# Optimization experiments

Measured on AMD Instinct MI355X. Metric: run time of the kernel, lower is better.

Reference implementation:

```python
import jax, jax.numpy as jnp
import numpy as np

BATCH = 8
HIDDEN = 256          # per-head size == input channels
NUM_HEADS = 9
H_IMG = 48
W_IMG = 48


def make_R(w, h):
    """Relative-position feature tensor R[i,j,k,l] = [dx, dy, dx^2, dy^2, dx*dy]
    with dx = k - i, dy = l - j (matches torch.meshgrid indexing='ij')."""
    gx, gy = jnp.meshgrid(jnp.arange(w), jnp.arange(h), indexing='ij')
    grid = jnp.stack([gx, gy], axis=-1).astype(jnp.float32)        # (w,h,2)
    rel = grid[None, None, :, :, :] - grid[:, :, None, None, :]    # (w,h,w,h,2)
    return jnp.concatenate(
        [rel, rel ** 2, (rel[..., 0] * rel[..., 1])[..., None]], axis=-1
    )                                                              # (w,h,w,h,5)


def setup_inputs() -> dict:
    key = jax.random.key(0)
    k1, k2, k3, k4, k5 = jax.random.split(key, 5)
    hidden_states = jax.random.normal(k1, (BATCH, HIDDEN, H_IMG, W_IMG), dtype=jnp.float32)
    # init per module: centers ~ N(0, init_mu_std=2.0), spreads = 1 + N(0, 0.01)
    attention_centers = 2.0 * jax.random.normal(k2, (NUM_HEADS, 2), dtype=jnp.float32)
    attention_spreads = 1.0 + 0.01 * jax.random.normal(k3, (NUM_HEADS,), dtype=jnp.float32)
    value_w = 0.02 * jax.random.normal(k4, (HIDDEN, NUM_HEADS * HIDDEN), dtype=jnp.float32)
    value_b = 0.02 * jax.random.normal(k5, (HIDDEN,), dtype=jnp.float32)
    return {
        'hidden_states': hidden_states,
        'attention_centers': attention_centers,
        'attention_spreads': attention_spreads,
        'value_w': value_w,
        'value_b': value_b,
    }


def reference(hidden_states, attention_centers, attention_spreads, value_w, value_b):
    b, c, h, w = hidden_states.shape
    x = jnp.transpose(hidden_states, (0, 3, 2, 1))  # (b, w, h, c)

    # heads target vectors (isotropic gaussian): a = c = sigma^2, b = 0
    a = attention_spreads ** 2                       # (H,)
    mu1 = attention_centers[:, 0]
    mu2 = attention_centers[:, 1]
    # t_h = -1/2 * [-2 a mu1, -2 a mu2, a, a, 0] = [a mu1, a mu2, -a/2, -a/2, 0]
    u = jnp.stack([a * mu1, a * mu2, -0.5 * a, -0.5 * a, jnp.zeros_like(a)], axis=-1)  # (H,5)

    R = make_R(w, h)                                               # (w,h,w,h,5)
    scores = jnp.einsum('ijkld,hd->ijhkl', R, u)                   # (w,h,H,w,h)
    probs = jax.nn.softmax(scores.reshape(w, h, NUM_HEADS, -1), axis=-1)
    probs = probs.reshape(w, h, NUM_HEADS, w, h)
    # dropout is identity in eval mode

    vals = jnp.einsum('ijhkl,bkld->bijhd', probs, x)               # (b,w,h,H,c)
    vals = vals.reshape(b, w, h, NUM_HEADS * c)
    out = vals @ value_w.T + value_b                               # (b,w,h,hidden)
    out = jnp.transpose(out, (0, 3, 2, 1))                         # (b,hidden,h,w)
    return out, probs
```

## Files before the change

### kernel.cpp

```cpp
#include <hip/hip_runtime.h>
#include <cstdint>
#include <cstddef>

#define SS    2304
#define OUT0  4718592

typedef short bf16x8 __attribute__((ext_vector_type(8)));
typedef float f32x4  __attribute__((ext_vector_type(4)));

__device__ __forceinline__ unsigned short f2bf(float f) {
    union { float f; unsigned int i; } v; v.f = f;
    unsigned int x = v.i;
    unsigned int r = x + 0x7fffu + ((x >> 16) & 1u);
    return (unsigned short)(r >> 16);
}

__global__ __launch_bounds__(256) void k_pre(const float* __restrict__ centers,
                                             const float* __restrict__ spreads,
                                             const float* __restrict__ hs,
                                             const float* __restrict__ Wv,
                                             float* __restrict__ p1, float* __restrict__ p2,
                                             unsigned short* __restrict__ p1b,
                                             unsigned short* __restrict__ p2b,
                                             unsigned short* __restrict__ hsb,
                                             unsigned short* __restrict__ WF) {
    int blk = blockIdx.x;
    int t = threadIdx.x;
    if (blk < 108) {
        int lane = t & 63, wave = t >> 6;
        int ridx = blk * 4 + wave;
        int h = ridx / 48, r = ridx % 48;
        float a = spreads[h]; a = a * a;
        float mu1 = centers[2 * h + 0];
        float mu2 = centers[2 * h + 1];
        bool act = lane < 48;
        float dx = (float)(lane - r);
        float q  = -0.5f * a * dx * dx;
        float g1 = act ? (a * mu1 * dx + q) : -INFINITY;
        float g2 = act ? (a * mu2 * dx + q) : -INFINITY;
        float m1 = g1, m2 = g2;
        #pragma unroll
        for (int off = 32; off >= 1; off >>= 1) {
            m1 = fmaxf(m1, __shfl_xor(m1, off));
            m2 = fmaxf(m2, __shfl_xor(m2, off));
        }
        float e1 = act ? expf(g1 - m1) : 0.f;
        float e2 = act ? expf(g2 - m2) : 0.f;
        float s1 = e1, s2 = e2;
        #pragma unroll
        for (int off = 32; off >= 1; off >>= 1) {
            s1 += __shfl_xor(s1, off);
            s2 += __shfl_xor(s2, off);
        }
        float v1 = e1 / s1, v2 = e2 / s2;
        if (act) {
            p1[h * SS + r * 48 + lane] = v1;
            p2[h * SS + r * 48 + lane] = v2;
        }
        p1b[(h * 48 + r) * 64 + lane] = act ? f2bf(v1) : 0;
        p2b[(h * 48 + r) * 64 + lane] = act ? f2bf(v2) : 0;
    } else if (blk < 396) {
        int kb = blk - 108;
        int e  = t;
        const float* src = Wv + (size_t)e * 2304 + kb * 8;
        float4 f0 = *(const float4*)src;
        float4 f1 = *(const float4*)(src + 4);
        uint4 o;
        o.x = (unsigned int)f2bf(f0.x) | ((unsigned int)f2bf(f0.y) << 16);
        o.y = (unsigned int)f2bf(f0.z) | ((unsigned int)f2bf(f0.w) << 16);
        o.z = (unsigned int)f2bf(f1.x) | ((unsigned int)f2bf(f1.y) << 16);
        o.w = (unsigned int)f2bf(f1.z) | ((unsigned int)f2bf(f1.w) << 16);
        *(uint4*)(WF + ((size_t)kb * 256 + e) * 8) = o;
    } else {
        int bd = blk - 396;
        const float* src = hs + (size_t)bd * SS;
        unsigned short* dst = hsb + (size_t)bd * 3072;
        for (int u = t; u < 384; u += 256) {
            int l = u >> 3, c8 = u & 7;
            uint4 o = {0u, 0u, 0u, 0u};
            if (c8 < 6) {
                const float* p = src + l * 48 + c8 * 8;
                float4 f0 = *(const float4*)p;
                float4 f1 = *(const float4*)(p + 4);
                o.x = (unsigned int)f2bf(f0.x) | ((unsigned int)f2bf(f0.y) << 16);
                o.y = (unsigned int)f2bf(f0.z) | ((unsigned int)f2bf(f0.w) << 16);
                o.z = (unsigned int)f2bf(f1.x) | ((unsigned int)f2bf(f1.y) << 16);
                o.w = (unsigned int)f2bf(f1.z) | ((unsigned int)f2bf(f1.w) << 16);
            }
            *(uint4*)(dst + l * 64 + c8 * 8) = o;
        }
    }
}

__global__ __launch_bounds__(256, 3) void k_attn(const unsigned short* __restrict__ hsb,
                                                 const unsigned short* __restrict__ p1b,
                                                 const unsigned short* __restrict__ p2b,
                                                 unsigned short* __restrict__ AF) {
    __shared__ unsigned short LSH[18432];

    int blk = blockIdx.x;
    int h = blk >> 8;
    int rem = blk & 255;
    int b = rem >> 5, od = rem & 31;
    int d0 = od * 8;
    int kb = h * 32 + od;

    int t = threadIdx.x;
    int lane = t & 63, wave = t >> 6;
    int l15 = lane & 15, quad = lane >> 4;

    const bf16x8* P1 = (const bf16x8*)(p1b + (size_t)h * 3072);
    const bf16x8* P2 = (const bf16x8*)(p2b + (size_t)h * 3072);
    bf16x8 pa[3][2], pb[3][2];
    #pragma unroll
    for (int tt = 0; tt < 3; ++tt)
        #pragma unroll
        for (int kt = 0; kt < 2; ++kt) {
            int u = (tt * 16 + l15) * 8 + kt * 4 + quad;
            pa[tt][kt] = P1[u];
            pb[tt][kt] = P2[u];
        }

    unsigned short* Sw = LSH + wave * 3456;
    for (int z = lane; z < 384; z += 64) {
        int row = z >> 3;
        *(unsigned int*)(Sw + row * 72 + 48 + ((z & 7) << 1)) = 0u;
    }

    f32x4 a2k[2][9];

    #pragma unroll
    for (int s = 0; s < 2; ++s) {
        int d = d0 + wave * 2 + s;
        size_t bd = (size_t)b * 256 + d;
        const bf16x8* X = (const bf16x8*)(hsb + bd * 3072);

        bf16x8 bx[3][2];
        #pragma unroll
        for (int lt = 0; lt < 3; ++lt)
            #pragma unroll
            for (int kt = 0; kt < 2; ++kt)
                bx[lt][kt] = X[(lt * 16 + l15) * 8 + kt * 4 + quad];

        f32x4 a1[9];
        #pragma unroll
        for (int q = 0; q < 9; ++q) a1[q] = (f32x4){0.f, 0.f, 0.f, 0.f};
        #pragma unroll
        for (int it = 0; it < 3; ++it)
            #pragma unroll
            for (int lt = 0; lt < 3; ++lt) {
                a1[it * 3 + lt] = __builtin_amdgcn_mfma_f32_16x16x32_bf16(
                    pa[it][0], bx[lt][0], a1[it * 3 + lt], 0, 0, 0);
                a1[it * 3 + lt] = __builtin_amdgcn_mfma_f32_16x16x32_bf16(
                    pa[it][1], bx[lt][1], a1[it * 3 + lt], 0, 0, 0);
            }

        #pragma unroll
        for (int it = 0; it < 3; ++it)
            #pragma unroll
            for (int lt = 0; lt < 3; ++lt)
                #pragma unroll
                for (int r = 0; r < 4; ++r)
                    Sw[(it * 16 + quad * 4 + r) * 72 + lt * 16 + l15] =
                        f2bf(a1[it * 3 + lt][r]);

        bf16x8 a2f[3][2];
        #pragma unroll
        for (int it = 0; it < 3; ++it)
            #pragma unroll
            for (int kt = 0; kt < 2; ++kt)
                a2f[it][kt] = *(const bf16x8*)(Sw + (it * 16 + l15) * 72 + kt * 32 + quad * 8);

        #pragma unroll
        for (int q = 0; q < 9; ++q) a2k[s][q] = (f32x4){0.f, 0.f, 0.f, 0.f};
        #pragma unroll
        for (int it = 0; it < 3; ++it)
            #pragma unroll
            for (int jt = 0; jt < 3; ++jt) {
                a2k[s][it * 3 + jt] = __builtin_amdgcn_mfma_f32_16x16x32_bf16(
                    a2f[it][0], pb[jt][0], a2k[s][it * 3 + jt], 0, 0, 0);
                a2k[s][it * 3 + jt] = __builtin_amdgcn_mfma_f32_16x16x32_bf16(
                    a2f[it][1], pb[jt][1], a2k[s][it * 3 + jt], 0, 0, 0);
            }
    }

    __syncthreads();
    #pragma unroll
    for (int s = 0; s < 2; ++s) {
        int kk = wave * 2 + s;
        #pragma unroll
        for (int it = 0; it < 3; ++it)
            #pragma unroll
            for (int jt = 0; jt < 3; ++jt) {
                f32x4 v = a2k[s][it * 3 + jt];
                unsigned int lo = (unsigned int)f2bf(v[0]) | ((unsigned int)f2bf(v[1]) << 16);
                unsigned int hi = (unsigned int)f2bf(v[2]) | ((unsigned int)f2bf(v[3]) << 16);
                int m = (jt * 16 + l15) * 48 + it * 16 + quad * 4;
                uint2 u2; u2.x = lo; u2.y = hi;
                *(uint2*)(LSH + kk * 2304 + m) = u2;
            }
    }
    __syncthreads();

    const uint2* Vr = (const uint2*)LSH;
    uint4* AFq = (uint4*)AF;
    size_t abase = (size_t)(b * 288 + kb) * 2304;
    for (int g = t; g < 576; g += 256) {
        uint2 rk[8];
        #pragma unroll
        for (int kk = 0; kk < 8; ++kk) rk[kk] = Vr[kk * 576 + g];
        #pragma unroll
        for (int mi = 0; mi < 4; ++mi) {
            unsigned int sel = (mi & 1) ? 0x07060302u : 0x05040100u;
            uint4 o;
            if (mi < 2) {
                o.x = __builtin_amdgcn_perm(rk[1].x, rk[0].x, sel);
                o.y = __builtin_amdgcn_perm(rk[3].x, rk[2].x, sel);
                o.z = __builtin_amdgcn_perm(rk[5].x, rk[4].x, sel);
                o.w = __builtin_amdgcn_perm(rk[7].x, rk[6].x, sel);
            } else {
                o.x = __builtin_amdgcn_perm(rk[1].y, rk[0].y, sel);
                o.y = __builtin_amdgcn_perm(rk[3].y, rk[2].y, sel);
                o.z = __builtin_amdgcn_perm(rk[5].y, rk[4].y, sel);
                o.w = __builtin_amdgcn_perm(rk[7].y, rk[6].y, sel);
            }
            AFq[abase + g * 4 + mi] = o;
        }
    }
}

__device__ __forceinline__ void probs_unit(int u, int t,
                                           const float* __restrict__ p1,
                                           const float* __restrict__ p2,
                                           float* __restrict__ probs) {
    #pragma unroll 2
    for (int tt = 0; tt < 8; ++tt) {
        int idx = u * 8 + tt;
        int h = idx % 9; int ij = idx / 9; int j = ij % 48; int i = ij / 48;
        const float* r1 = p1 + (h * 48 + i) * 48;
        const float4* r2 = (const float4*)(p2 + (h * 48 + j) * 48);
        f32x4* op = (f32x4*)(probs + (size_t)idx * SS);
        for (int g = t; g < 576; g += 256) {
            int k = g / 12, lq = g % 12;
            float s = r1[k];
            float4 q = r2[lq];
            f32x4 v; v[0] = s * q.x; v[1] = s * q.y; v[2] = s * q.z; v[3] = s * q.w;
            __builtin_nontemporal_store(v, op + g);
        }
    }
}

__global__ __launch_bounds__(256) void k_tail(const unsigned short* __restrict__ AF,
                                              const unsigned short* __restrict__ WF,
                                              const float* __restrict__ vb,
                                              float* __restrict__ out,
                                              const float* __restrict__ p1,
                                              const float* __restrict__ p2,
                                              float* __restrict__ probs) {
    int blk = blockIdx.x;
    int t = threadIdx.x;

    if (blk >= 576) {
        probs_unit(blk - 576, t, p1, p2, probs);
        return;
    }

    int b = blk / 72, mb = blk % 72;
    int lane = t & 63, wave = t >> 6;
    int l15 = lane & 15, quad = lane >> 4;
    int m0 = mb * 32;
    int e0 = wave * 64;

    const bf16x8* pa = (const bf16x8*)AF + (size_t)b * 288 * 2304
                       + (size_t)quad * 2304 + m0 + l15;
    const bf16x8* pw = (const bf16x8*)WF + (size_t)quad * 256 + e0 + l15;

    f32x4 acc[2][4];
    #pragma unroll
    for (int i = 0; i < 2; i++)
        #pragma unroll
        for (int j = 0; j < 4; j++) acc[i][j] = (f32x4){0.f, 0.f, 0.f, 0.f};

    bf16x8 a_cur[2], w_cur[4], a_nxt[2], w_nxt[4];
    a_cur[0] = pa[0];  a_cur[1] = pa[16];
    w_cur[0] = pw[0];  w_cur[1] = pw[16]; w_cur[2] = pw[32]; w_cur[3] = pw[48];

    for (int c = 0; c < 72; ++c) {
        if (c < 71) {
            a_nxt[0] = pa[9216];      a_nxt[1] = pa[9216 + 16];
            w_nxt[0] = pw[1024];      w_nxt[1] = pw[1024 + 16];
            w_nxt[2] = pw[1024 + 32]; w_nxt[3] = pw[1024 + 48];
        }
        #pragma unroll
        for (int tm = 0; tm < 2; ++tm)
            #pragma unroll
            for (int te = 0; te < 4; ++te)
                acc[tm][te] = __builtin_amdgcn_mfma_f32_16x16x32_bf16(
                    a_cur[tm], w_cur[te], acc[tm][te], 0, 0, 0);
        a_cur[0] = a_nxt[0]; a_cur[1] = a_nxt[1];
        w_cur[0] = w_nxt[0]; w_cur[1] = w_nxt[1]; w_cur[2] = w_nxt[2]; w_cur[3] = w_nxt[3];
        pa += 9216; pw += 1024;
    }

    size_t obase = (size_t)b * 589824;
    #pragma unroll
    for (int te = 0; te < 4; ++te) {
        int e = e0 + te * 16 + l15;
        float bias = vb[e];
        #pragma unroll
        for (int tm = 0; tm < 2; ++tm) {
            int m = m0 + tm * 16 + quad * 4;
            float4 v;
            v.x = acc[tm][te][0] + bias;
            v.y = acc[tm][te][1] + bias;
            v.z = acc[tm][te][2] + bias;
            v.w = acc[tm][te][3] + bias;
            *(float4*)(out + obase + (size_t)e * SS + m) = v;
        }
    }
}

__global__ __launch_bounds__(256) void k_probs_sep(const float* __restrict__ p1,
                                                   const float* __restrict__ p2,
                                                   float* __restrict__ probs) {
    probs_unit(blockIdx.x, threadIdx.x, p1, p2, probs);
}

extern "C" void kernel_launch(void* const* d_in, const int* in_sizes, int n_in,
                              void* d_out, int out_size, void* d_ws, size_t ws_size,
                              hipStream_t stream) {
    const float* hs      = (const float*)d_in[0];
    const float* centers = (const float*)d_in[1];
    const float* spreads = (const float*)d_in[2];
    const float* Wv      = (const float*)d_in[3];
    const float* vbias   = (const float*)d_in[4];

    float* out   = (float*)d_out;
    float* probs = out + OUT0;

    const size_t needBig = 99000000;
    bool big = ws_size >= needBig;

    unsigned short *AF, *WF, *hsb, *p1b, *p2b;
    float *p1, *p2;
    if (big) {
        unsigned short* w = (unsigned short*)d_ws;
        AF  = w;
        WF  = AF + 42467328;
        hsb = WF + 589824;
        p1b = hsb + 6291456;
        p2b = p1b + 27648;
        p1  = (float*)(p2b + 27648);
        p2  = p1 + 20736;
    } else {
        p1  = (float*)d_ws;
        p2  = p1 + 20736;
        p1b = (unsigned short*)(p2 + 20736);
        p2b = p1b + 27648;
        AF  = (unsigned short*)probs;
        WF  = AF + 42467328;
        hsb = WF + 589824;
    }

    k_pre<<<2444, 256, 0, stream>>>(centers, spreads, hs, Wv, p1, p2, p1b, p2b, hsb, WF);
    k_attn<<<2304, 256, 0, stream>>>(hsb, p1b, p2b, AF);
    if (big) {
        k_tail<<<576 + 2592, 256, 0, stream>>>(AF, WF, vbias, out, p1, p2, probs);
    } else {
        k_tail<<<576, 256, 0, stream>>>(AF, WF, vbias, out, p1, p2, probs);
        k_probs_sep<<<2592, 256, 0, stream>>>(p1, p2, probs);
    }
}
```

Baseline: 305.0 us.

## Fuse hidden-state bf16 conversion into attention kernel and move weight conversion there

Removes the separate hs-to-bf16 staging buffer. k_attn now loads fp32 hidden states directly and converts them to bf16 in registers, zero-padding the unused k columns. The Wv-to-bf16 conversion blocks move from k_pre into extra blocks appended to the k_attn grid, so k_pre only computes the small softmax tables. This removes a full write-then-read pass over the hidden states and shrinks the workspace requirement. The cost is twice the load bytes per element in k_attn and redundant conversion work, since each hs row is read by several heads and blocks.

```diff
diff --git a/kernel.cpp b/kernel.cpp
--- a/kernel.cpp
+++ b/kernel.cpp
@@ -17,52 +17,58 @@
 
 __global__ __launch_bounds__(256) void k_pre(const float* __restrict__ centers,
                                              const float* __restrict__ spreads,
-                                             const float* __restrict__ hs,
-                                             const float* __restrict__ Wv,
                                              float* __restrict__ p1, float* __restrict__ p2,
                                              unsigned short* __restrict__ p1b,
-                                             unsigned short* __restrict__ p2b,
-                                             unsigned short* __restrict__ hsb,
-                                             unsigned short* __restrict__ WF) {
+                                             unsigned short* __restrict__ p2b) {
+    int t = threadIdx.x;
+    int lane = t & 63, wave = t >> 6;
+    int ridx = blockIdx.x * 4 + wave;
+    int h = ridx / 48, r = ridx % 48;
+    float a = spreads[h]; a = a * a;
+    float mu1 = centers[2 * h + 0];
+    float mu2 = centers[2 * h + 1];
+    bool act = lane < 48;
+    float dx = (float)(lane - r);
+    float q  = -0.5f * a * dx * dx;
+    float g1 = act ? (a * mu1 * dx + q) : -INFINITY;
+    float g2 = act ? (a * mu2 * dx + q) : -INFINITY;
+    float m1 = g1, m2 = g2;
+    #pragma unroll
+    for (int off = 32; off >= 1; off >>= 1) {
+        m1 = fmaxf(m1, __shfl_xor(m1, off));
+        m2 = fmaxf(m2, __shfl_xor(m2, off));
+    }
+    float e1 = act ? expf(g1 - m1) : 0.f;
+    float e2 = act ? expf(g2 - m2) : 0.f;
+    float s1 = e1, s2 = e2;
+    #pragma unroll
+    for (int off = 32; off >= 1; off >>= 1) {
+        s1 += __shfl_xor(s1, off);
+        s2 += __shfl_xor(s2, off);
+    }
+    float v1 = e1 / s1, v2 = e2 / s2;
+    if (act) {
+        p1[h * SS + r * 48 + lane] = v1;
+        p2[h * SS + r * 48 + lane] = v2;
+    }
+    p1b[(h * 48 + r) * 64 + lane] = act ? f2bf(v1) : 0;
+    p2b[(h * 48 + r) * 64 + lane] = act ? f2bf(v2) : 0;
+}
+
+__global__ __launch_bounds__(256, 3) void k_attn(const float* __restrict__ hs,
+                                                 const unsigned short* __restrict__ p1b,
+                                                 const unsigned short* __restrict__ p2b,
+                                                 unsigned short* __restrict__ AF,
+                                                 const float* __restrict__ Wv,
+                                                 unsigned short* __restrict__ WF) {
+    __shared__ unsigned short LSH[18432];
+
     int blk = blockIdx.x;
     int t = threadIdx.x;
-    if (blk < 108) {
-        int lane = t & 63, wave = t >> 6;
-        int ridx = blk * 4 + wave;
-        int h = ridx / 48, r = ridx % 48;
-        float a = spreads[h]; a = a * a;
-        float mu1 = centers[2 * h + 0];
-        float mu2 = centers[2 * h + 1];
-        bool act = lane < 48;
-        float dx = (float)(lane - r);
-        float q  = -0.5f * a * dx * dx;
-        float g1 = act ? (a * mu1 * dx + q) : -INFINITY;
-        float g2 = act ? (a * mu2 * dx + q) : -INFINITY;
-        float m1 = g1, m2 = g2;
-        #pragma unroll
-        for (int off = 32; off >= 1; off >>= 1) {
-            m1 = fmaxf(m1, __shfl_xor(m1, off));
-            m2 = fmaxf(m2, __shfl_xor(m2, off));
-        }
-        float e1 = act ? expf(g1 - m1) : 0.f;
-        float e2 = act ? expf(g2 - m2) : 0.f;
-        float s1 = e1, s2 = e2;
-        #pragma unroll
-        for (int off = 32; off >= 1; off >>= 1) {
-            s1 += __shfl_xor(s1, off);
-            s2 += __shfl_xor(s2, off);
-        }
-        float v1 = e1 / s1, v2 = e2 / s2;
-        if (act) {
-            p1[h * SS + r * 48 + lane] = v1;
-            p2[h * SS + r * 48 + lane] = v2;
-        }
-        p1b[(h * 48 + r) * 64 + lane] = act ? f2bf(v1) : 0;
-        p2b[(h * 48 + r) * 64 + lane] = act ? f2bf(v2) : 0;
-    } else if (blk < 396) {
-        int kb = blk - 108;
-        int e  = t;
-        const float* src = Wv + (size_t)e * 2304 + kb * 8;
+
+    if (blk >= 2304) {
+        int kb = blk - 2304;
+        const float* src = Wv + (size_t)t * 2304 + kb * 8;
         float4 f0 = *(const float4*)src;
         float4 f1 = *(const float4*)(src + 4);
         uint4 o;
@@ -70,42 +76,16 @@
         o.y = (unsigned int)f2bf(f0.z) | ((unsigned int)f2bf(f0.w) << 16);
         o.z = (unsigned int)f2bf(f1.x) | ((unsigned int)f2bf(f1.y) << 16);
         o.w = (unsigned int)f2bf(f1.z) | ((unsigned int)f2bf(f1.w) << 16);
-        *(uint4*)(WF + ((size_t)kb * 256 + e) * 8) = o;
-    } else {
-        int bd = blk - 396;
-        const float* src = hs + (size_t)bd * SS;
-        unsigned short* dst = hsb + (size_t)bd * 3072;
-        for (int u = t; u < 384; u += 256) {
-            int l = u >> 3, c8 = u & 7;
-            uint4 o = {0u, 0u, 0u, 0u};
-            if (c8 < 6) {
-                const float* p = src + l * 48 + c8 * 8;
-                float4 f0 = *(const float4*)p;
-                float4 f1 = *(const float4*)(p + 4);
-                o.x = (unsigned int)f2bf(f0.x) | ((unsigned int)f2bf(f0.y) << 16);
-                o.y = (unsigned int)f2bf(f0.z) | ((unsigned int)f2bf(f0.w) << 16);
-                o.z = (unsigned int)f2bf(f1.x) | ((unsigned int)f2bf(f1.y) << 16);
-                o.w = (unsigned int)f2bf(f1.z) | ((unsigned int)f2bf(f1.w) << 16);
-            }
-            *(uint4*)(dst + l * 64 + c8 * 8) = o;
-        }
-    }
-}
-
-__global__ __launch_bounds__(256, 3) void k_attn(const unsigned short* __restrict__ hsb,
-                                                 const unsigned short* __restrict__ p1b,
-                                                 const unsigned short* __restrict__ p2b,
-                                                 unsigned short* __restrict__ AF) {
-    __shared__ unsigned short LSH[18432];
-
-    int blk = blockIdx.x;
+        *(uint4*)(WF + ((size_t)kb * 256 + t) * 8) = o;
+        return;
+    }
+
     int h = blk >> 8;
     int rem = blk & 255;
     int b = rem >> 5, od = rem & 31;
     int d0 = od * 8;
     int kb = h * 32 + od;
 
-    int t = threadIdx.x;
     int lane = t & 63, wave = t >> 6;
     int l15 = lane & 15, quad = lane >> 4;
 
@@ -133,14 +113,25 @@
     for (int s = 0; s < 2; ++s) {
         int d = d0 + wave * 2 + s;
         size_t bd = (size_t)b * 256 + d;
-        const bf16x8* X = (const bf16x8*)(hsb + bd * 3072);
+        const float* X = hs + bd * SS;
 
         bf16x8 bx[3][2];
         #pragma unroll
         for (int lt = 0; lt < 3; ++lt)
             #pragma unroll
-            for (int kt = 0; kt < 2; ++kt)
-                bx[lt][kt] = X[(lt * 16 + l15) * 8 + kt * 4 + quad];
+            for (int kt = 0; kt < 2; ++kt) {
+                bf16x8 r = {0, 0, 0, 0, 0, 0, 0, 0};
+                if (kt == 0 || quad < 2) {
+                    const float* px = X + (lt * 16 + l15) * 48 + kt * 32 + quad * 8;
+                    float4 f0 = *(const float4*)px;
+                    float4 f1 = *(const float4*)(px + 4);
+                    r[0] = (short)f2bf(f0.x); r[1] = (short)f2bf(f0.y);
+                    r[2] = (short)f2bf(f0.z); r[3] = (short)f2bf(f0.w);
+                    r[4] = (short)f2bf(f1.x); r[5] = (short)f2bf(f1.y);
+                    r[6] = (short)f2bf(f1.z); r[7] = (short)f2bf(f1.w);
+                }
+                bx[lt][kt] = r;
+            }
 
         f32x4 a1[9];
         #pragma unroll
@@ -338,17 +329,16 @@
     float* out   = (float*)d_out;
     float* probs = out + OUT0;
 
-    const size_t needBig = 99000000;
+    const size_t needBig = 87000000;
     bool big = ws_size >= needBig;
 
-    unsigned short *AF, *WF, *hsb, *p1b, *p2b;
+    unsigned short *AF, *WF, *p1b, *p2b;
     float *p1, *p2;
     if (big) {
         unsigned short* w = (unsigned short*)d_ws;
         AF  = w;
         WF  = AF + 42467328;
-        hsb = WF + 589824;
-        p1b = hsb + 6291456;
+        p1b = WF + 589824;
         p2b = p1b + 27648;
         p1  = (float*)(p2b + 27648);
         p2  = p1 + 20736;
@@ -359,11 +349,10 @@
         p2b = p1b + 27648;
         AF  = (unsigned short*)probs;
         WF  = AF + 42467328;
-        hsb = WF + 589824;
-    }
-
-    k_pre<<<2444, 256, 0, stream>>>(centers, spreads, hs, Wv, p1, p2, p1b, p2b, hsb, WF);
-    k_attn<<<2304, 256, 0, stream>>>(hsb, p1b, p2b, AF);
+    }
+
+    k_pre<<<108, 256, 0, stream>>>(centers, spreads, p1, p2, p1b, p2b);
+    k_attn<<<2304 + 288, 256, 0, stream>>>(hs, p1b, p2b, AF, Wv, WF);
     if (big) {
         k_tail<<<576 + 2592, 256, 0, stream>>>(AF, WF, vbias, out, p1, p2, probs);
     } else {
```

After: 304.7 us. No clear change (-0.1%).
